# Performance work log

Hardware: AMD Instinct MI355X
Metric: run time of the kernel (lower is better)

The kernel has to match this reference:

```python
import jax, jax.numpy as jnp
import numpy as np

N = 524288
L = 16          # num_levels
F = 2           # per_level_dim
T = 1 << 19     # hashmap size per level
BASE, MAXR = 32, 2048
SCALE = np.exp(np.log(MAXR / BASE) / (L - 1))
RES = [int(np.floor(BASE * SCALE ** lv)) + 1 for lv in range(L)]
ACTIVE = 4 * F  # init_active_level * per_level_dim (progressive mask)
D_HID = 64
N_FREQS = 6

_P1 = jnp.uint32(2654435761)
_P2 = jnp.uint32(805459861)
_OFF = jnp.array([[(c >> d) & 1 for d in range(3)] for c in range(8)], dtype=jnp.uint32)  # [8,3]


def setup_inputs() -> dict:
    key = jax.random.key(0)
    ks = jax.random.split(key, 8)
    x = (jax.random.uniform(ks[0], (N, 3)) * 2.0 - 1.0) * 0.999  # inside [-bound, bound]
    v = jax.random.normal(ks[1], (N, 3))
    v = v / jnp.linalg.norm(v, axis=-1, keepdims=True)
    o = jax.random.normal(ks[2], (N, 3))  # unused by forward (kept for signature fidelity)
    table = jax.random.uniform(ks[3], (L, T, F), minval=-1e-4, maxval=1e-4)
    d_in = 3 + 3 * 2 * N_FREQS + L * F  # xyz + fourier + hashgrid = 71
    def lin(k, fi, fo):
        return jax.random.normal(k, (fi, fo)) * np.sqrt(2.0 / fi).astype(np.float32)
    dw1 = lin(ks[4], d_in, D_HID); db1 = jnp.zeros((D_HID,), jnp.float32)
    dw2 = lin(ks[5], D_HID, 1 + D_HID); db2 = jnp.zeros((1 + D_HID,), jnp.float32)
    rw1 = lin(ks[6], D_HID + 9, D_HID); rb1 = jnp.zeros((D_HID,), jnp.float32)
    rw2 = lin(ks[7], D_HID, 3); rb2 = jnp.zeros((3,), jnp.float32)
    return dict(x=x, v=v, o=o, table=table, dw1=dw1, db1=db1, dw2=dw2, db2=db2,
                rw1=rw1, rb1=rb1, rw2=rw2, rb2=rb2)


def hashgrid(x01, table):
    """Multi-res hash encoding with Smoothstep interpolation. x01 in [0,1]^3."""
    feats = []
    for lv in range(L):
        pos = x01 * RES[lv]
        p0 = jnp.floor(pos)
        t = pos - p0
        w = t * t * (3.0 - 2.0 * t)                       # smoothstep weights [N,3]
        corner = p0.astype(jnp.uint32)[:, None, :] + _OFF[None]  # [N,8,3]
        h = (corner[..., 0] ^ (corner[..., 1] * _P1) ^ (corner[..., 2] * _P2)) & jnp.uint32(T - 1)
        cw = jnp.prod(jnp.where(_OFF[None] == 1, w[:, None, :], 1.0 - w[:, None, :]), axis=-1)  # [N,8]
        feats.append(jnp.sum(table[lv][h.astype(jnp.int32)] * cw[..., None], axis=1))  # [N,F]
    return jnp.concatenate(feats, axis=-1)  # [N, L*F]


def fourier(x):
    freqs = 2.0 ** jnp.arange(N_FREQS, dtype=x.dtype)  # log-sampled 2^0..2^5
    ang = x[..., None] * freqs                         # [N,3,6]
    return jnp.concatenate([jnp.sin(ang), jnp.cos(ang)], axis=-1).reshape(x.shape[0], -1)


def sh3(d):
    """Spherical harmonics, degree 3 (levels=3) -> 9 features."""
    xx, yy, zz = d[..., 0], d[..., 1], d[..., 2]
    return jnp.stack([
        0.28209479177387814 * jnp.ones_like(xx),
        -0.4886025119029199 * yy, 0.4886025119029199 * zz, -0.4886025119029199 * xx,
        1.0925484305920792 * xx * yy, -1.0925484305920792 * yy * zz,
        0.9461746957575601 * zz * zz - 0.31539156525252005,
        -1.0925484305920792 * xx * zz,
        0.5462742152960396 * (xx * xx - yy * yy)], axis=-1)


def reference(x, v, o, table, dw1, db1, dw2, db2, rw1, rb1, rw2, rb2):
    x01 = (x + 1.0) * 0.5  # bound = 1.0
    grid = hashgrid(x01, table)
    mask = (jnp.arange(L * F) < ACTIVE).astype(grid.dtype)  # progressive level mask
    x_enc = jnp.concatenate([x, fourier(x), grid * mask], axis=-1)  # [N,71]
    h = jax.nn.relu(x_enc @ dw1 + db1)
    dout = h @ dw2 + db2                 # [N, 1 + d_hidden]
    sigma = jnp.exp(dout[..., :1])       # trunc_exp forward == exp
    feat = jax.nn.relu(dout[..., 1:])
    rgb_in = jnp.concatenate([feat, sh3(v)], axis=-1)  # [N, 73]
    hr = jax.nn.relu(rgb_in @ rw1 + rb1)
    rgb = jax.nn.sigmoid(hr @ rw2 + rb2)
    return sigma, rgb
```

## Files before the change

kernel.cpp:

```cpp
#include <hip/hip_runtime.h>

#define NPTS   524288
#define TBLM   ((1u << 19) - 1u)
#define THR    256
#define CHUNK  128
#define CHUNKS 4
#define GRID   (NPTS / (CHUNK * CHUNKS))

typedef _Float16 half8  __attribute__((ext_vector_type(8)));
typedef _Float16 half4v __attribute__((ext_vector_type(4)));
typedef float    f32x4  __attribute__((ext_vector_type(4)));


__global__ __launch_bounds__(256)
void prep(const float* __restrict__ dw1, const float* __restrict__ db1,
          const float* __restrict__ dw2, const float* __restrict__ db2,
          const float* __restrict__ rw1, const float* __restrict__ rb1,
          const float* __restrict__ rw2, const float* __restrict__ rb2,
          void* __restrict__ ws)
{
    const int t = blockIdx.x * 256 + threadIdx.x;
    if (t < 16384) {
        float w = 0.0f;
        if (t < 4096) {
            const int u = t, mkc = u >> 9, m = mkc >> 1, kc = mkc & 1;
            const int lane = (u >> 3) & 63, j = u & 7;
            const int row = 16 * m + (lane & 15);
            const int kp  = kc * 32 + (lane >> 4) * 8 + j;
            if (kp < 39)      w = dw1[kp * 64 + row];
            else if (kp == 39) w = 0.0f;
            else if (kp < 48) w = dw1[(kp - 1) * 64 + row];
        } else if (t < 9216) {
            const int u = t - 4096, mkc = u >> 9, m = mkc >> 1, kc = mkc & 1;
            const int lane = (u >> 3) & 63, j = u & 7;
            const int row = 16 * m + (lane & 15);
            const int k   = kc * 32 + (lane >> 4) * 8 + j;
            if (row < 65) w = dw2[k * 65 + row];
        } else if (t < 15360) {
            const int u = t - 9216, mkc = u >> 9, m = mkc / 3, kc = mkc - 3 * m;
            const int lane = (u >> 3) & 63, j = u & 7;
            const int row = 16 * m + (lane & 15);
            const int kp  = kc * 32 + (lane >> 4) * 8 + j;
            if (kp >= 1 && kp <= 73) w = rw1[(kp - 1) * 64 + row];
        } else {
            const int u = t - 15360, kc = u >> 9;
            const int lane = (u >> 3) & 63, j = u & 7;
            const int row = lane & 15;
            const int k   = kc * 32 + (lane >> 4) * 8 + j;
            if (row < 3) w = rw2[k * 3 + row];
        }
        ((_Float16*)ws)[t] = (_Float16)w;
    } else if (t < 16384 + 224) {
        const int u = t - 16384;
        float b = 0.0f;
        if (u < 64)        b = db1[u];
        else if (u < 144)  { const int r = u - 64;  if (r < 65) b = db2[r]; }
        else if (u < 208)  b = rb1[u - 144];
        else               { const int r = u - 208; if (r < 3)  b = rb2[r]; }
        ((float*)((char*)ws + 32768))[u] = b;
    }
}

__device__ __forceinline__ float sstep(float t) { return t * t * (3.0f - 2.0f * t); }

__global__ __launch_bounds__(THR, 2)
void nerf_fwd(const float* __restrict__ x,
              const float* __restrict__ v,
              const float* __restrict__ table,
              const float* __restrict__ ws,
              float* __restrict__ out)
{
    __shared__ __align__(16) unsigned char smem[78720];
    _Float16* wt    = (_Float16*)smem;
    float*    sbias = (float*)(smem + 32768);
    _Float16* aB    = (_Float16*)(smem + 33664);
    _Float16* bB    = (_Float16*)(smem + 60288);

    const int tid  = threadIdx.x;
    const int lane = tid & 63;
    const int wv   = tid >> 6;
    const int lr   = lane & 15;
    const int lg   = lane >> 4;

    {
        const uint4* src = (const uint4*)ws;
        uint4* dst = (uint4*)smem;
        #pragma unroll
        for (int i = 0; i < 9; ++i) {
            const int idx = tid + i * THR;
            if (idx < 2104) dst[idx] = src[idx];
        }
    }
    __syncthreads();

    const int gi0 = blockIdx.x * (CHUNK * CHUNKS);

    for (int c = 0; c < CHUNKS; ++c) {
        const int cbase = gi0 + c * CHUNK;

        {
            const int p  = (wv << 5) + (lane >> 1);
            const int gi = cbase + p;
            _Float16* row = aB + p * 104;
            const float x0 = x[3 * gi + 0], x1 = x[3 * gi + 1], x2 = x[3 * gi + 2];
            if (lane & 1) {
                const float u0 = (x0 + 1.0f) * 0.5f, u1 = (x1 + 1.0f) * 0.5f, u2 = (x2 + 1.0f) * 0.5f;
                const float resf[4] = {33.0f, 43.0f, 56.0f, 74.0f};
                float g[8];
                #pragma unroll
                for (int lv = 0; lv < 4; ++lv) {
                    const float px = u0 * resf[lv], py = u1 * resf[lv], pz = u2 * resf[lv];
                    const float fx = floorf(px), fy = floorf(py), fz = floorf(pz);
                    const float wx = sstep(px - fx), wy = sstep(py - fy), wz = sstep(pz - fz);
                    const unsigned cx = (unsigned)fx, cy = (unsigned)fy, cz = (unsigned)fz;
                    float g0 = 0.f, g1 = 0.f;
                    #pragma unroll
                    for (int cc = 0; cc < 8; ++cc) {
                        const unsigned hx = cx + (cc & 1);
                        const unsigned hy = cy + ((cc >> 1) & 1);
                        const unsigned hz = cz + ((cc >> 2) & 1);
                        const unsigned hh = (hx ^ (hy * 2654435761u) ^ (hz * 805459861u)) & TBLM;
                        const float2 tv = *reinterpret_cast<const float2*>(
                            table + ((unsigned)lv * (TBLM + 1u) + hh) * 2u);
                        const float cw = ((cc & 1) ? wx : 1.0f - wx) *
                                         ((cc & 2) ? wy : 1.0f - wy) *
                                         ((cc & 4) ? wz : 1.0f - wz);
                        g0 = fmaf(cw, tv.x, g0);
                        g1 = fmaf(cw, tv.y, g1);
                    }
                    g[2 * lv]     = g0;
                    g[2 * lv + 1] = g1;
                }
                half8 h;
                #pragma unroll
                for (int i = 0; i < 8; ++i) h[i] = (_Float16)g[i];
                *(half8*)(row + 40) = h;
                const float v0 = v[3 * gi + 0], v1 = v[3 * gi + 1], v2 = v[3 * gi + 2];
                float sh[9];
                sh[0] = 0.28209479177387814f;
                sh[1] = -0.4886025119029199f * v1;
                sh[2] =  0.4886025119029199f * v2;
                sh[3] = -0.4886025119029199f * v0;
                sh[4] =  1.0925484305920792f * v0 * v1;
                sh[5] = -1.0925484305920792f * v1 * v2;
                sh[6] =  0.9461746957575601f * v2 * v2 - 0.31539156525252005f;
                sh[7] = -1.0925484305920792f * v0 * v2;
                sh[8] =  0.5462742152960396f * (v0 * v0 - v1 * v1);
                half8 s0, s1, z;
                s0[0] = (_Float16)0.f;
                #pragma unroll
                for (int i = 0; i < 7; ++i) s0[i + 1] = (_Float16)sh[i];
                s1[0] = (_Float16)sh[7]; s1[1] = (_Float16)sh[8];
                #pragma unroll
                for (int i = 2; i < 8; ++i) s1[i] = (_Float16)0.f;
                #pragma unroll
                for (int i = 0; i < 8; ++i) z[i] = (_Float16)0.f;
                *(half8*)(row + 64) = s0;
                *(half8*)(row + 72) = s1;
                *(half8*)(row + 80) = z;
                *(half8*)(row + 88) = z;
            } else {
                float e[40];
                e[0] = x0; e[1] = x1; e[2] = x2;
                const float a[3] = {x0, x1, x2};
                #pragma unroll
                for (int d = 0; d < 3; ++d)
                    #pragma unroll
                    for (int f = 0; f < 6; ++f) {
                        const float ang = a[d] * (float)(1 << f);
                        e[3 + d * 12 + f]     = __sinf(ang);
                        e[3 + d * 12 + 6 + f] = __cosf(ang);
                    }
                e[39] = 0.0f;
                #pragma unroll
                for (int chk = 0; chk < 5; ++chk) {
                    half8 h;
                    #pragma unroll
                    for (int i = 0; i < 8; ++i) h[i] = (_Float16)e[chk * 8 + i];
                    *(half8*)(row + chk * 8) = h;
                }
                half8 z;
                #pragma unroll
                for (int i = 0; i < 8; ++i) z[i] = (_Float16)0.f;
                *(half8*)(row + 48) = z;
                *(half8*)(row + 56) = z;
            }
        }

        {
            half8 A[4][2];
            #pragma unroll
            for (int m = 0; m < 4; ++m)
                #pragma unroll
                for (int kc = 0; kc < 2; ++kc)
                    A[m][kc] = *(const half8*)(wt + (m * 2 + kc) * 512 + lane * 8);
            #pragma unroll
            for (int n = 0; n < 2; ++n) {
                const int pt = (wv << 5) + (n << 4) + lr;
                const half8 B0 = *(const half8*)(aB + pt * 104 + 0 * 32 + lg * 8);
                const half8 B1 = *(const half8*)(aB + pt * 104 + 1 * 32 + lg * 8);
                #pragma unroll
                for (int m = 0; m < 4; ++m) {
                    f32x4 cr = *(const f32x4*)(sbias + 0 + m * 16 + 4 * lg);
                    cr = __builtin_amdgcn_mfma_f32_16x16x32_f16(A[m][0], B0, cr, 0, 0, 0);
                    cr = __builtin_amdgcn_mfma_f32_16x16x32_f16(A[m][1], B1, cr, 0, 0, 0);
                    half4v o4;
                    #pragma unroll
                    for (int r = 0; r < 4; ++r) o4[r] = (_Float16)fmaxf(cr[r], 0.f);
                    *(half4v*)(bB + pt * 72 + 16 * m + 4 * lg) = o4;
                }
            }
        }

        {
            half8 A[5][2];
            #pragma unroll
            for (int m = 0; m < 5; ++m)
                #pragma unroll
                for (int kc = 0; kc < 2; ++kc)
                    A[m][kc] = *(const half8*)(wt + 4096 + (m * 2 + kc) * 512 + lane * 8);
            #pragma unroll
            for (int n = 0; n < 2; ++n) {
                const int pt = (wv << 5) + (n << 4) + lr;
                const half8 B0 = *(const half8*)(bB + pt * 72 + 0 * 32 + lg * 8);
                const half8 B1 = *(const half8*)(bB + pt * 72 + 1 * 32 + lg * 8);
                #pragma unroll
                for (int m = 0; m < 4; ++m) {
                    f32x4 cr = *(const f32x4*)(sbias + 64 + m * 16 + 4 * lg);
                    cr = __builtin_amdgcn_mfma_f32_16x16x32_f16(A[m][0], B0, cr, 0, 0, 0);
                    cr = __builtin_amdgcn_mfma_f32_16x16x32_f16(A[m][1], B1, cr, 0, 0, 0);
                    half4v o4;
                    #pragma unroll
                    for (int r = 0; r < 4; ++r) o4[r] = (_Float16)fmaxf(cr[r], 0.f);
                    *(half4v*)(aB + pt * 104 + 16 * m + 4 * lg) = o4;
                    if (m == 0 && lg == 0)
                        out[cbase + pt] = __expf(cr[0]);
                }
                {
                    f32x4 cr = *(const f32x4*)(sbias + 64 + 4 * 16 + 4 * lg);
                    cr = __builtin_amdgcn_mfma_f32_16x16x32_f16(A[4][0], B0, cr, 0, 0, 0);
                    cr = __builtin_amdgcn_mfma_f32_16x16x32_f16(A[4][1], B1, cr, 0, 0, 0);
                    if (lg == 0) aB[pt * 104 + 64] = (_Float16)fmaxf(cr[0], 0.f);
                }
            }
        }

        {
            half8 A[4][3];
            #pragma unroll
            for (int m = 0; m < 4; ++m)
                #pragma unroll
                for (int kc = 0; kc < 3; ++kc)
                    A[m][kc] = *(const half8*)(wt + 9216 + (m * 3 + kc) * 512 + lane * 8);
            #pragma unroll
            for (int n = 0; n < 2; ++n) {
                const int pt = (wv << 5) + (n << 4) + lr;
                const half8 B0 = *(const half8*)(aB + pt * 104 + 0 * 32 + lg * 8);
                const half8 B1 = *(const half8*)(aB + pt * 104 + 1 * 32 + lg * 8);
                const half8 B2 = *(const half8*)(aB + pt * 104 + 2 * 32 + lg * 8);
                #pragma unroll
                for (int m = 0; m < 4; ++m) {
                    f32x4 cr = *(const f32x4*)(sbias + 144 + m * 16 + 4 * lg);
                    cr = __builtin_amdgcn_mfma_f32_16x16x32_f16(A[m][0], B0, cr, 0, 0, 0);
                    cr = __builtin_amdgcn_mfma_f32_16x16x32_f16(A[m][1], B1, cr, 0, 0, 0);
                    cr = __builtin_amdgcn_mfma_f32_16x16x32_f16(A[m][2], B2, cr, 0, 0, 0);
                    half4v o4;
                    #pragma unroll
                    for (int r = 0; r < 4; ++r) o4[r] = (_Float16)fmaxf(cr[r], 0.f);
                    *(half4v*)(bB + pt * 72 + 16 * m + 4 * lg) = o4;
                }
            }
        }

        {
            const half8 A0 = *(const half8*)(wt + 15360 + 0 * 512 + lane * 8);
            const half8 A1 = *(const half8*)(wt + 15360 + 1 * 512 + lane * 8);
            #pragma unroll
            for (int n = 0; n < 2; ++n) {
                const int pt = (wv << 5) + (n << 4) + lr;
                const half8 B0 = *(const half8*)(bB + pt * 72 + 0 * 32 + lg * 8);
                const half8 B1 = *(const half8*)(bB + pt * 72 + 1 * 32 + lg * 8);
                f32x4 cr = *(const f32x4*)(sbias + 208 + 4 * lg);
                cr = __builtin_amdgcn_mfma_f32_16x16x32_f16(A0, B0, cr, 0, 0, 0);
                cr = __builtin_amdgcn_mfma_f32_16x16x32_f16(A1, B1, cr, 0, 0, 0);
                if (lg == 0) {
                    const int gpt = cbase + pt;
                    #pragma unroll
                    for (int r = 0; r < 3; ++r)
                        out[NPTS + 3 * gpt + r] = 1.0f / (1.0f + __expf(-cr[r]));
                }
            }
        }
    }
}

extern "C" void kernel_launch(void* const* d_in, const int* in_sizes, int n_in,
                              void* d_out, int out_size, void* d_ws, size_t ws_size,
                              hipStream_t stream) {
    const float* x     = (const float*)d_in[0];
    const float* v     = (const float*)d_in[1];
    const float* table = (const float*)d_in[3];
    const float* dw1   = (const float*)d_in[4];
    const float* db1   = (const float*)d_in[5];
    const float* dw2   = (const float*)d_in[6];
    const float* db2   = (const float*)d_in[7];
    const float* rw1   = (const float*)d_in[8];
    const float* rb1   = (const float*)d_in[9];
    const float* rw2   = (const float*)d_in[10];
    const float* rb2   = (const float*)d_in[11];
    float* out = (float*)d_out;

    hipLaunchKernelGGL(prep, dim3(65), dim3(256), 0, stream,
                       dw1, db1, dw2, db2, rw1, rb1, rw2, rb2, d_ws);
    hipLaunchKernelGGL(nerf_fwd, dim3(GRID), dim3(THR), 0, stream,
                       x, v, table, (const float*)d_ws, out);
}
```

Before: 191.6 us.

## Double block threads to 512 and split per-point encoding across four lanes

The block grows from 256 to 512 threads, so each wave now handles 16 points per chunk instead of 32. Point encoding is split over four lanes: one does the Fourier features, two each gather two hash-grid levels, and one does the spherical harmonics and zero padding. The MLP stages drop the n-loop and reload weight fragments from LDS for each m tile instead of holding them in registers. The aim is more latency hiding for the random table gathers through finer split and higher occupancy, at the cost of more LDS weight reads per MFMA and a tighter register budget under launch_bounds(512,4).

```diff
diff --git a/kernel.cpp b/kernel.cpp
--- a/kernel.cpp
+++ b/kernel.cpp
@@ -2,7 +2,7 @@
 
 #define NPTS   524288
 #define TBLM   ((1u << 19) - 1u)
-#define THR    256
+#define THR    512
 #define CHUNK  128
 #define CHUNKS 4
 #define GRID   (NPTS / (CHUNK * CHUNKS))
@@ -63,7 +63,7 @@
 
 __device__ __forceinline__ float sstep(float t) { return t * t * (3.0f - 2.0f * t); }
 
-__global__ __launch_bounds__(THR, 2)
+__global__ __launch_bounds__(THR, 4)
 void nerf_fwd(const float* __restrict__ x,
               const float* __restrict__ v,
               const float* __restrict__ table,
@@ -86,7 +86,7 @@
         const uint4* src = (const uint4*)ws;
         uint4* dst = (uint4*)smem;
         #pragma unroll
-        for (int i = 0; i < 9; ++i) {
+        for (int i = 0; i < 5; ++i) {
             const int idx = tid + i * THR;
             if (idx < 2104) dst[idx] = src[idx];
         }
@@ -99,42 +99,11 @@
         const int cbase = gi0 + c * CHUNK;
 
         {
-            const int p  = (wv << 5) + (lane >> 1);
-            const int gi = cbase + p;
+            const int p    = (wv << 4) + (lane >> 2);
+            const int gi   = cbase + p;
+            const int role = lane & 3;
             _Float16* row = aB + p * 104;
-            const float x0 = x[3 * gi + 0], x1 = x[3 * gi + 1], x2 = x[3 * gi + 2];
-            if (lane & 1) {
-                const float u0 = (x0 + 1.0f) * 0.5f, u1 = (x1 + 1.0f) * 0.5f, u2 = (x2 + 1.0f) * 0.5f;
-                const float resf[4] = {33.0f, 43.0f, 56.0f, 74.0f};
-                float g[8];
-                #pragma unroll
-                for (int lv = 0; lv < 4; ++lv) {
-                    const float px = u0 * resf[lv], py = u1 * resf[lv], pz = u2 * resf[lv];
-                    const float fx = floorf(px), fy = floorf(py), fz = floorf(pz);
-                    const float wx = sstep(px - fx), wy = sstep(py - fy), wz = sstep(pz - fz);
-                    const unsigned cx = (unsigned)fx, cy = (unsigned)fy, cz = (unsigned)fz;
-                    float g0 = 0.f, g1 = 0.f;
-                    #pragma unroll
-                    for (int cc = 0; cc < 8; ++cc) {
-                        const unsigned hx = cx + (cc & 1);
-                        const unsigned hy = cy + ((cc >> 1) & 1);
-                        const unsigned hz = cz + ((cc >> 2) & 1);
-                        const unsigned hh = (hx ^ (hy * 2654435761u) ^ (hz * 805459861u)) & TBLM;
-                        const float2 tv = *reinterpret_cast<const float2*>(
-                            table + ((unsigned)lv * (TBLM + 1u) + hh) * 2u);
-                        const float cw = ((cc & 1) ? wx : 1.0f - wx) *
-                                         ((cc & 2) ? wy : 1.0f - wy) *
-                                         ((cc & 4) ? wz : 1.0f - wz);
-                        g0 = fmaf(cw, tv.x, g0);
-                        g1 = fmaf(cw, tv.y, g1);
-                    }
-                    g[2 * lv]     = g0;
-                    g[2 * lv + 1] = g1;
-                }
-                half8 h;
-                #pragma unroll
-                for (int i = 0; i < 8; ++i) h[i] = (_Float16)g[i];
-                *(half8*)(row + 40) = h;
+            if (role == 3) {
                 const float v0 = v[3 * gi + 0], v1 = v[3 * gi + 1], v2 = v[3 * gi + 2];
                 float sh[9];
                 sh[0] = 0.28209479177387814f;
@@ -155,140 +124,153 @@
                 for (int i = 2; i < 8; ++i) s1[i] = (_Float16)0.f;
                 #pragma unroll
                 for (int i = 0; i < 8; ++i) z[i] = (_Float16)0.f;
+                *(half8*)(row + 48) = z;
+                *(half8*)(row + 56) = z;
                 *(half8*)(row + 64) = s0;
                 *(half8*)(row + 72) = s1;
                 *(half8*)(row + 80) = z;
                 *(half8*)(row + 88) = z;
             } else {
-                float e[40];
-                e[0] = x0; e[1] = x1; e[2] = x2;
-                const float a[3] = {x0, x1, x2};
-                #pragma unroll
-                for (int d = 0; d < 3; ++d)
-                    #pragma unroll
-                    for (int f = 0; f < 6; ++f) {
-                        const float ang = a[d] * (float)(1 << f);
-                        e[3 + d * 12 + f]     = __sinf(ang);
-                        e[3 + d * 12 + 6 + f] = __cosf(ang);
+                const float x0 = x[3 * gi + 0], x1 = x[3 * gi + 1], x2 = x[3 * gi + 2];
+                if (role == 0) {
+                    float e[40];
+                    e[0] = x0; e[1] = x1; e[2] = x2;
+                    const float a[3] = {x0, x1, x2};
+                    #pragma unroll
+                    for (int d = 0; d < 3; ++d)
+                        #pragma unroll
+                        for (int f = 0; f < 6; ++f) {
+                            const float ang = a[d] * (float)(1 << f);
+                            e[3 + d * 12 + f]     = __sinf(ang);
+                            e[3 + d * 12 + 6 + f] = __cosf(ang);
+                        }
+                    e[39] = 0.0f;
+                    #pragma unroll
+                    for (int chk = 0; chk < 5; ++chk) {
+                        half8 h;
+                        #pragma unroll
+                        for (int i = 0; i < 8; ++i) h[i] = (_Float16)e[chk * 8 + i];
+                        *(half8*)(row + chk * 8) = h;
                     }
-                e[39] = 0.0f;
-                #pragma unroll
-                for (int chk = 0; chk < 5; ++chk) {
-                    half8 h;
-                    #pragma unroll
-                    for (int i = 0; i < 8; ++i) h[i] = (_Float16)e[chk * 8 + i];
-                    *(half8*)(row + chk * 8) = h;
+                } else {
+                    const float u0 = (x0 + 1.0f) * 0.5f, u1 = (x1 + 1.0f) * 0.5f, u2 = (x2 + 1.0f) * 0.5f;
+                    const float rfA = (role == 1) ? 33.0f : 56.0f;
+                    const float rfB = (role == 1) ? 43.0f : 74.0f;
+                    const unsigned lvA = (role == 1) ? 0u : 2u;
+                    float g[4];
+                    #pragma unroll
+                    for (int s = 0; s < 2; ++s) {
+                        const float rf = s ? rfB : rfA;
+                        const unsigned lv = lvA + (unsigned)s;
+                        const float px = u0 * rf, py = u1 * rf, pz = u2 * rf;
+                        const float fx = floorf(px), fy = floorf(py), fz = floorf(pz);
+                        const float wx = sstep(px - fx), wy = sstep(py - fy), wz = sstep(pz - fz);
+                        const unsigned cx = (unsigned)fx, cy = (unsigned)fy, cz = (unsigned)fz;
+                        float g0 = 0.f, g1 = 0.f;
+                        #pragma unroll
+                        for (int cc = 0; cc < 8; ++cc) {
+                            const unsigned hx = cx + (cc & 1);
+                            const unsigned hy = cy + ((cc >> 1) & 1);
+                            const unsigned hz = cz + ((cc >> 2) & 1);
+                            const unsigned hh = (hx ^ (hy * 2654435761u) ^ (hz * 805459861u)) & TBLM;
+                            const float2 tv = *reinterpret_cast<const float2*>(
+                                table + (lv * (TBLM + 1u) + hh) * 2u);
+                            const float cw = ((cc & 1) ? wx : 1.0f - wx) *
+                                             ((cc & 2) ? wy : 1.0f - wy) *
+                                             ((cc & 4) ? wz : 1.0f - wz);
+                            g0 = fmaf(cw, tv.x, g0);
+                            g1 = fmaf(cw, tv.y, g1);
+                        }
+                        g[2 * s]     = g0;
+                        g[2 * s + 1] = g1;
+                    }
+                    half4v h4;
+                    #pragma unroll
+                    for (int i = 0; i < 4; ++i) h4[i] = (_Float16)g[i];
+                    *(half4v*)(row + 40 + (role - 1) * 4) = h4;
                 }
-                half8 z;
-                #pragma unroll
-                for (int i = 0; i < 8; ++i) z[i] = (_Float16)0.f;
-                *(half8*)(row + 48) = z;
-                *(half8*)(row + 56) = z;
-            }
-        }
-
-        {
-            half8 A[4][2];
+            }
+        }
+
+        const int pt = (wv << 4) + lr;
+
+        {
+            const half8 B0 = *(const half8*)(aB + pt * 104 + 0 * 32 + lg * 8);
+            const half8 B1 = *(const half8*)(aB + pt * 104 + 1 * 32 + lg * 8);
             #pragma unroll
-            for (int m = 0; m < 4; ++m)
-                #pragma unroll
-                for (int kc = 0; kc < 2; ++kc)
-                    A[m][kc] = *(const half8*)(wt + (m * 2 + kc) * 512 + lane * 8);
+            for (int m = 0; m < 4; ++m) {
+                const half8 A0 = *(const half8*)(wt + (m * 2 + 0) * 512 + lane * 8);
+                const half8 A1 = *(const half8*)(wt + (m * 2 + 1) * 512 + lane * 8);
+                f32x4 cr = *(const f32x4*)(sbias + 0 + m * 16 + 4 * lg);
+                cr = __builtin_amdgcn_mfma_f32_16x16x32_f16(A0, B0, cr, 0, 0, 0);
+                cr = __builtin_amdgcn_mfma_f32_16x16x32_f16(A1, B1, cr, 0, 0, 0);
+                half4v o4;
+                #pragma unroll
+                for (int r = 0; r < 4; ++r) o4[r] = (_Float16)fmaxf(cr[r], 0.f);
+                *(half4v*)(bB + pt * 72 + 16 * m + 4 * lg) = o4;
+            }
+        }
+
+        {
+            const half8 B0 = *(const half8*)(bB + pt * 72 + 0 * 32 + lg * 8);
+            const half8 B1 = *(const half8*)(bB + pt * 72 + 1 * 32 + lg * 8);
             #pragma unroll
-            for (int n = 0; n < 2; ++n) {
-                const int pt = (wv << 5) + (n << 4) + lr;
-                const half8 B0 = *(const half8*)(aB + pt * 104 + 0 * 32 + lg * 8);
-                const half8 B1 = *(const half8*)(aB + pt * 104 + 1 * 32 + lg * 8);
-                #pragma unroll
-                for (int m = 0; m < 4; ++m) {
-                    f32x4 cr = *(const f32x4*)(sbias + 0 + m * 16 + 4 * lg);
-                    cr = __builtin_amdgcn_mfma_f32_16x16x32_f16(A[m][0], B0, cr, 0, 0, 0);
-                    cr = __builtin_amdgcn_mfma_f32_16x16x32_f16(A[m][1], B1, cr, 0, 0, 0);
-                    half4v o4;
-                    #pragma unroll
-                    for (int r = 0; r < 4; ++r) o4[r] = (_Float16)fmaxf(cr[r], 0.f);
-                    *(half4v*)(bB + pt * 72 + 16 * m + 4 * lg) = o4;
-                }
-            }
-        }
-
-        {
-            half8 A[5][2];
+            for (int m = 0; m < 4; ++m) {
+                const half8 A0 = *(const half8*)(wt + 4096 + (m * 2 + 0) * 512 + lane * 8);
+                const half8 A1 = *(const half8*)(wt + 4096 + (m * 2 + 1) * 512 + lane * 8);
+                f32x4 cr = *(const f32x4*)(sbias + 64 + m * 16 + 4 * lg);
+                cr = __builtin_amdgcn_mfma_f32_16x16x32_f16(A0, B0, cr, 0, 0, 0);
+                cr = __builtin_amdgcn_mfma_f32_16x16x32_f16(A1, B1, cr, 0, 0, 0);
+                half4v o4;
+                #pragma unroll
+                for (int r = 0; r < 4; ++r) o4[r] = (_Float16)fmaxf(cr[r], 0.f);
+                *(half4v*)(aB + pt * 104 + 16 * m + 4 * lg) = o4;
+                if (m == 0 && lg == 0)
+                    out[cbase + pt] = __expf(cr[0]);
+            }
+            {
+                const half8 A0 = *(const half8*)(wt + 4096 + (4 * 2 + 0) * 512 + lane * 8);
+                const half8 A1 = *(const half8*)(wt + 4096 + (4 * 2 + 1) * 512 + lane * 8);
+                f32x4 cr = *(const f32x4*)(sbias + 64 + 4 * 16 + 4 * lg);
+                cr = __builtin_amdgcn_mfma_f32_16x16x32_f16(A0, B0, cr, 0, 0, 0);
+                cr = __builtin_amdgcn_mfma_f32_16x16x32_f16(A1, B1, cr, 0, 0, 0);
+                if (lg == 0) aB[pt * 104 + 64] = (_Float16)fmaxf(cr[0], 0.f);
+            }
+        }
+
+        {
+            const half8 B0 = *(const half8*)(aB + pt * 104 + 0 * 32 + lg * 8);
+            const half8 B1 = *(const half8*)(aB + pt * 104 + 1 * 32 + lg * 8);
+            const half8 B2 = *(const half8*)(aB + pt * 104 + 2 * 32 + lg * 8);
             #pragma unroll
-            for (int m = 0; m < 5; ++m)
-                #pragma unroll
-                for (int kc = 0; kc < 2; ++kc)
-                    A[m][kc] = *(const half8*)(wt + 4096 + (m * 2 + kc) * 512 + lane * 8);
-            #pragma unroll
-            for (int n = 0; n < 2; ++n) {
-                const int pt = (wv << 5) + (n << 4) + lr;
-                const half8 B0 = *(const half8*)(bB + pt * 72 + 0 * 32 + lg * 8);
-                const half8 B1 = *(const half8*)(bB + pt * 72 + 1 * 32 + lg * 8);
-                #pragma unroll
-                for (int m = 0; m < 4; ++m) {
-                    f32x4 cr = *(const f32x4*)(sbias + 64 + m * 16 + 4 * lg);
-                    cr = __builtin_amdgcn_mfma_f32_16x16x32_f16(A[m][0], B0, cr, 0, 0, 0);
-                    cr = __builtin_amdgcn_mfma_f32_16x16x32_f16(A[m][1], B1, cr, 0, 0, 0);
-                    half4v o4;
-                    #pragma unroll
-                    for (int r = 0; r < 4; ++r) o4[r] = (_Float16)fmaxf(cr[r], 0.f);
-                    *(half4v*)(aB + pt * 104 + 16 * m + 4 * lg) = o4;
-                    if (m == 0 && lg == 0)
-                        out[cbase + pt] = __expf(cr[0]);
-                }
-                {
-                    f32x4 cr = *(const f32x4*)(sbias + 64 + 4 * 16 + 4 * lg);
-                    cr = __builtin_amdgcn_mfma_f32_16x16x32_f16(A[4][0], B0, cr, 0, 0, 0);
-                    cr = __builtin_amdgcn_mfma_f32_16x16x32_f16(A[4][1], B1, cr, 0, 0, 0);
-                    if (lg == 0) aB[pt * 104 + 64] = (_Float16)fmaxf(cr[0], 0.f);
-                }
-            }
-        }
-
-        {
-            half8 A[4][3];
-            #pragma unroll
-            for (int m = 0; m < 4; ++m)
-                #pragma unroll
-                for (int kc = 0; kc < 3; ++kc)
-                    A[m][kc] = *(const half8*)(wt + 9216 + (m * 3 + kc) * 512 + lane * 8);
-            #pragma unroll
-            for (int n = 0; n < 2; ++n) {
-                const int pt = (wv << 5) + (n << 4) + lr;
-                const half8 B0 = *(const half8*)(aB + pt * 104 + 0 * 32 + lg * 8);
-                const half8 B1 = *(const half8*)(aB + pt * 104 + 1 * 32 + lg * 8);
-                const half8 B2 = *(const half8*)(aB + pt * 104 + 2 * 32 + lg * 8);
-                #pragma unroll
-                for (int m = 0; m < 4; ++m) {
-                    f32x4 cr = *(const f32x4*)(sbias + 144 + m * 16 + 4 * lg);
-                    cr = __builtin_amdgcn_mfma_f32_16x16x32_f16(A[m][0], B0, cr, 0, 0, 0);
-                    cr = __builtin_amdgcn_mfma_f32_16x16x32_f16(A[m][1], B1, cr, 0, 0, 0);
-                    cr = __builtin_amdgcn_mfma_f32_16x16x32_f16(A[m][2], B2, cr, 0, 0, 0);
-                    half4v o4;
-                    #pragma unroll
-                    for (int r = 0; r < 4; ++r) o4[r] = (_Float16)fmaxf(cr[r], 0.f);
-                    *(half4v*)(bB + pt * 72 + 16 * m + 4 * lg) = o4;
-                }
+            for (int m = 0; m < 4; ++m) {
+                const half8 A0 = *(const half8*)(wt + 9216 + (m * 3 + 0) * 512 + lane * 8);
+                const half8 A1 = *(const half8*)(wt + 9216 + (m * 3 + 1) * 512 + lane * 8);
+                const half8 A2 = *(const half8*)(wt + 9216 + (m * 3 + 2) * 512 + lane * 8);
+                f32x4 cr = *(const f32x4*)(sbias + 144 + m * 16 + 4 * lg);
+                cr = __builtin_amdgcn_mfma_f32_16x16x32_f16(A0, B0, cr, 0, 0, 0);
+                cr = __builtin_amdgcn_mfma_f32_16x16x32_f16(A1, B1, cr, 0, 0, 0);
+                cr = __builtin_amdgcn_mfma_f32_16x16x32_f16(A2, B2, cr, 0, 0, 0);
+                half4v o4;
+                #pragma unroll
+                for (int r = 0; r < 4; ++r) o4[r] = (_Float16)fmaxf(cr[r], 0.f);
+                *(half4v*)(bB + pt * 72 + 16 * m + 4 * lg) = o4;
             }
         }
 
         {
             const half8 A0 = *(const half8*)(wt + 15360 + 0 * 512 + lane * 8);
             const half8 A1 = *(const half8*)(wt + 15360 + 1 * 512 + lane * 8);
-            #pragma unroll
-            for (int n = 0; n < 2; ++n) {
-                const int pt = (wv << 5) + (n << 4) + lr;
-                const half8 B0 = *(const half8*)(bB + pt * 72 + 0 * 32 + lg * 8);
-                const half8 B1 = *(const half8*)(bB + pt * 72 + 1 * 32 + lg * 8);
-                f32x4 cr = *(const f32x4*)(sbias + 208 + 4 * lg);
-                cr = __builtin_amdgcn_mfma_f32_16x16x32_f16(A0, B0, cr, 0, 0, 0);
-                cr = __builtin_amdgcn_mfma_f32_16x16x32_f16(A1, B1, cr, 0, 0, 0);
-                if (lg == 0) {
-                    const int gpt = cbase + pt;
-                    #pragma unroll
-                    for (int r = 0; r < 3; ++r)
-                        out[NPTS + 3 * gpt + r] = 1.0f / (1.0f + __expf(-cr[r]));
-                }
+            const half8 B0 = *(const half8*)(bB + pt * 72 + 0 * 32 + lg * 8);
+            const half8 B1 = *(const half8*)(bB + pt * 72 + 1 * 32 + lg * 8);
+            f32x4 cr = *(const f32x4*)(sbias + 208 + 4 * lg);
+            cr = __builtin_amdgcn_mfma_f32_16x16x32_f16(A0, B0, cr, 0, 0, 0);
+            cr = __builtin_amdgcn_mfma_f32_16x16x32_f16(A1, B1, cr, 0, 0, 0);
+            if (lg == 0) {
+                const int gpt = cbase + pt;
+                #pragma unroll
+                for (int r = 0; r < 3; ++r)
+                    out[NPTS + 3 * gpt + r] = 1.0f / (1.0f + __expf(-cr[r]));
             }
         }
     }
```

New measurement: 191.5 us. Within noise of the previous version (-0.1%).
